# Optimization experiments

Hardware: AMD Instinct MI355X
Metric: run time of the kernel (lower is better)

The kernel has to match this reference:

```python
import jax, jax.numpy as jnp
import numpy as np

N, C_IN, C_OUT, K, S, P, H, W = 16, 64, 128, 3, 1, 1, 224, 224

def setup_inputs() -> dict:
    key = jax.random.key(0)
    kx, kw = jax.random.split(key)
    x = jax.random.normal(kx, (N, C_IN, H, W), dtype=jnp.float32)
    weight = jax.random.normal(kw, (C_OUT, C_IN, K, K), dtype=jnp.float32)
    bias = jnp.zeros((C_OUT,), dtype=jnp.float32)
    return {"x": x, "weight": weight, "bias": bias}

def reference(x, weight, bias):
    # im2col + matmul with stride 1 is exactly a standard conv2d with SAME-style padding P
    out = jax.lax.conv_general_dilated(
        x, weight,
        window_strides=(S, S),
        padding=((P, P), (P, P)),
        dimension_numbers=("NCHW", "OIHW", "NCHW"),
    )
    return out + bias[None, :, None, None]  # [N, C_OUT, H, W]
```

## Files before the change

kernel.cpp:

```cpp
#include <hip/hip_runtime.h>
#include <cstdint>
#include <cstddef>


typedef short bf16x8 __attribute__((ext_vector_type(8)));
typedef float f32x4 __attribute__((ext_vector_type(4)));

#define N_ 16
#define CI_ 64
#define CO_ 128
#define H_ 224
#define W_ 224
#define HW_ (H_ * W_)

#define WP_ 226
#define CBS_ 1808ULL
#define HPS_ 14464ULL
#define NS_ 3268864ULL

__device__ __forceinline__ unsigned short f2bf(float f) {
    unsigned u = __builtin_bit_cast(unsigned, f);
    u += 0x7FFFu + ((u >> 16) & 1u);
    return (unsigned short)(u >> 16);
}

__global__ void prep_weight(const float* __restrict__ w, unsigned short* __restrict__ wr) {
    int i = blockIdx.x * 256 + threadIdx.x;
    if (i >= 9 * CO_ * CI_) return;
    int ci = i & 63;
    int co = (i >> 6) & 127;
    int t  = i >> 13;
    wr[i] = f2bf(w[(co * CI_ + ci) * 9 + t]);
}

__global__ __launch_bounds__(256) void prep_x(const float* __restrict__ x,
                                              unsigned short* __restrict__ xp) {
    int b = blockIdx.x;
    int n = b / 226, hp = b - n * 226;
    int tid = threadIdx.x;
    unsigned short* row = xp + (size_t)n * NS_ + (size_t)hp * HPS_;
    if (hp == 0 || hp == 225) {
        #pragma unroll
        for (int k = 0; k < 8; ++k) {
            int i = k * 256 + tid;
            if (i < 1808) ((uint4*)row)[i] = make_uint4(0, 0, 0, 0);
        }
        return;
    }
    int h = hp - 1;
    const float* xb = x + (size_t)n * CI_ * HW_ + (size_t)h * W_;
    for (int k = 0; k < 7; ++k) {
        int item = k * 256 + tid;
        int w = item % 224;
        int cb = item / 224;
        unsigned r[4];
        #pragma unroll
        for (int c = 0; c < 4; ++c) {
            float lo = xb[(size_t)(cb * 8 + 2 * c) * HW_ + w];
            float hi = xb[(size_t)(cb * 8 + 2 * c + 1) * HW_ + w];
            r[c] = (unsigned)f2bf(lo) | ((unsigned)f2bf(hi) << 16);
        }
        *(uint4*)(row + (size_t)cb * CBS_ + (size_t)(w + 1) * 8) = make_uint4(r[0], r[1], r[2], r[3]);
    }
    if (tid < 16) {
        int cb = tid >> 1, wp = (tid & 1) * 225;
        *(uint4*)(row + (size_t)cb * CBS_ + (size_t)wp * 8) = make_uint4(0, 0, 0, 0);
    }
}

__global__ __launch_bounds__(512, 2) void conv2(
    const unsigned short* __restrict__ xp, const unsigned short* __restrict__ wr,
    const float* __restrict__ bias, float* __restrict__ out)
{
    __shared__ __align__(16) unsigned short xs[4 * 4 * 226 * 8];

    int bid = blockIdx.x;
    int swz = (bid & 7) * 224 + (bid >> 3);
    int n = swz / 112;
    int hblk = swz - n * 112;
    int h0 = hblk * 2;

    int tid = threadIdx.x, lane = tid & 63, wid = tid >> 6;
    int hr = wid & 1, nh = (wid >> 1) & 1, mh = wid >> 2;
    int lrow = lane & 15, lk = lane >> 4;

    f32x4 acc[4][7];
    #pragma unroll
    for (int a = 0; a < 4; ++a)
        #pragma unroll
        for (int b2 = 0; b2 < 7; ++b2)
            #pragma unroll
            for (int k = 0; k < 4; ++k)
                acc[a][b2][k] = 0.0f;

    const unsigned short* xpn = xp + (size_t)n * NS_;

    for (int ch = 0; ch < 2; ++ch) {
        if (ch) __syncthreads();
        #pragma unroll
        for (int rr = 0; rr < 2; ++rr) {
            int run = wid * 2 + rr;
            int r = run >> 2, cbl = run & 3;
            const unsigned short* src = xpn + (size_t)(h0 + r) * HPS_ + (size_t)(ch * 4 + cbl) * CBS_;
            unsigned short* dst = &xs[(size_t)(r * 4 + cbl) * (226 * 8)];
            #pragma unroll
            for (int c = 0; c < 4; ++c) {
                int chunk = c * 64 + lane;
                if (chunk < 226)
                    __builtin_amdgcn_global_load_lds(
                        (const __attribute__((address_space(1))) void*)(src + (size_t)chunk * 8),
                        (__attribute__((address_space(3))) void*)(dst + c * 512),
                        16, 0, 0);
            }
        }
        __syncthreads();

        #pragma unroll
        for (int t = 0; t < 9; ++t) {
            int kh = t / 3, kw = t - kh * 3;
            bf16x8 afr[4];
            #pragma unroll
            for (int mf = 0; mf < 4; ++mf) {
                size_t ai = ((size_t)(t * 128 + mh * 64 + mf * 16 + lrow)) * 64
                          + (size_t)(ch * 32 + lk * 8);
                afr[mf] = *(const bf16x8*)(wr + ai);
            }
            int rbase = ((hr + kh) * 4 + lk) * 226;
            int wpb = nh * 112 + lrow + kw;
            #pragma unroll
            for (int nf = 0; nf < 7; ++nf) {
                bf16x8 bfr = *(const bf16x8*)(&xs[(size_t)(rbase + wpb + nf * 16) * 8]);
                #pragma unroll
                for (int mf = 0; mf < 4; ++mf)
                    acc[mf][nf] = __builtin_amdgcn_mfma_f32_16x16x32_bf16(
                        afr[mf], bfr, acc[mf][nf], 0, 0, 0);
            }
        }
    }

    __syncthreads();
    float* lf = (float*)xs;
    int h = h0 + hr;
    #pragma unroll
    for (int mf = 0; mf < 4; ++mf) {
        float bv[4];
        #pragma unroll
        for (int r = 0; r < 4; ++r)
            bv[r] = bias[mh * 64 + mf * 16 + lk * 4 + r];
        float* wbase = lf + wid * 1808 + lk * 452 + lrow;
        #pragma unroll
        for (int r = 0; r < 4; ++r)
            #pragma unroll
            for (int nf = 0; nf < 7; ++nf)
                wbase[r * 112 + nf * 16] = acc[mf][nf][r] + bv[r];
        #pragma unroll
        for (int j = 0; j < 7; ++j) {
            int idx4 = j * 64 + lane;
            int col = idx4 / 28;
            int w4  = idx4 - col * 28;
            f32x4 v = *(const f32x4*)(lf + wid * 1808 + (col >> 2) * 452 + (col & 3) * 112 + w4 * 4);
            size_t ob = (((size_t)n * CO_ + mh * 64 + mf * 16 + col) * H_ + h) * W_
                      + nh * 112 + w4 * 4;
            *(f32x4*)(out + ob) = v;
        }
    }
}

__global__ __launch_bounds__(512, 2) void conv_mfma(
    const float* __restrict__ x, const unsigned short* __restrict__ wr,
    const float* __restrict__ bias, float* __restrict__ out)
{
    __shared__ unsigned short xs[4 * 4 * 226 * 8];
    int bid = blockIdx.x;
    int swz = (bid & 7) * 224 + (bid >> 3);
    int n = swz / 112;
    int hblk = swz - n * 112;
    int h0 = hblk * 2;
    int tid = threadIdx.x;
    int lane = tid & 63;
    int wid = tid >> 6;
    int hr = wid & 1, nh = (wid >> 1) & 1, mh = wid >> 2;
    int lrow = lane & 15, lk = lane >> 4;

    f32x4 acc[4][7];
    #pragma unroll
    for (int a = 0; a < 4; ++a)
        #pragma unroll
        for (int b = 0; b < 7; ++b)
            #pragma unroll
            for (int k = 0; k < 4; ++k)
                acc[a][b][k] = 0.0f;

    for (int ch = 0; ch < 2; ++ch) {
        if (ch) __syncthreads();
        const float* xb = x + ((size_t)n * CI_ + (size_t)ch * 32) * HW_;
        int wcol = tid % 224;
        int rem = tid / 224;
        for (int it = 0; it < 7; ++it) {
            float v[8]; int bi[8];
            #pragma unroll
            for (int u = 0; u < 8; ++u) {
                int ciL = rem & 31;
                int r4 = rem >> 5;
                int hh = h0 - 1 + r4;
                float val = 0.0f;
                if ((unsigned)hh < (unsigned)H_)
                    val = xb[(size_t)ciL * HW_ + (size_t)hh * W_ + wcol];
                v[u] = val;
                bi[u] = (((r4 << 2) + (ciL >> 3)) * 226 + wcol + 1) * 8 + (ciL & 7);
                wcol += 64; rem += 2;
                if (wcol >= 224) { wcol -= 224; rem += 1; }
            }
            #pragma unroll
            for (int u = 0; u < 8; ++u)
                xs[bi[u]] = f2bf(v[u]);
        }
        if (tid < 256) {
            int wp = (tid & 1) * 225;
            int ciL = (tid >> 1) & 31;
            int r4 = tid >> 6;
            xs[(((r4 << 2) + (ciL >> 3)) * 226 + wp) * 8 + (ciL & 7)] = 0;
        }
        __syncthreads();

        #pragma unroll
        for (int t = 0; t < 9; ++t) {
            int kh = t / 3, kw = t - kh * 3;
            bf16x8 afr[4];
            #pragma unroll
            for (int mf = 0; mf < 4; ++mf) {
                size_t ai = ((size_t)(t * 128 + mh * 64 + mf * 16 + lrow)) * 64
                          + (size_t)(ch * 32 + lk * 8);
                afr[mf] = *(const bf16x8*)(wr + ai);
            }
            int rbase = ((hr + kh) * 4 + lk) * 226;
            int wpb = nh * 112 + lrow + kw;
            #pragma unroll
            for (int nf = 0; nf < 7; ++nf) {
                bf16x8 bfr = *(const bf16x8*)(&xs[(size_t)(rbase + wpb + nf * 16) * 8]);
                #pragma unroll
                for (int mf = 0; mf < 4; ++mf)
                    acc[mf][nf] = __builtin_amdgcn_mfma_f32_16x16x32_bf16(
                        afr[mf], bfr, acc[mf][nf], 0, 0, 0);
            }
        }
    }

    int h = h0 + hr;
    #pragma unroll
    for (int mf = 0; mf < 4; ++mf) {
        #pragma unroll
        for (int r = 0; r < 4; ++r) {
            int co = mh * 64 + mf * 16 + lk * 4 + r;
            float bv = bias[co];
            size_t ob = (((size_t)n * CO_ + co) * H_ + h) * W_ + nh * 112 + lrow;
            #pragma unroll
            for (int nf = 0; nf < 7; ++nf)
                out[ob + (size_t)nf * 16] = acc[mf][nf][r] + bv;
        }
    }
}

extern "C" void kernel_launch(void* const* d_in, const int* in_sizes, int n_in,
                              void* d_out, int out_size, void* d_ws, size_t ws_size,
                              hipStream_t stream) {
    const float* x    = (const float*)d_in[0];
    const float* w    = (const float*)d_in[1];
    const float* bias = (const float*)d_in[2];
    float* out = (float*)d_out;
    unsigned short* wr = (unsigned short*)d_ws;
    const size_t xp_bytes = (size_t)N_ * NS_ * 2;
    const size_t need = 147456 + xp_bytes;

    prep_weight<<<dim3(288), dim3(256), 0, stream>>>(w, wr);
    if (ws_size >= need) {
        unsigned short* xp = wr + 73728;
        prep_x<<<dim3(16 * 226), dim3(256), 0, stream>>>(x, xp);
        conv2<<<dim3(16 * 112), dim3(512), 0, stream>>>(xp, wr, bias, out);
    } else {
        conv_mfma<<<dim3(16 * 112), dim3(512), 0, stream>>>(x, wr, bias, out);
    }
}
```

Baseline: 287.6 us.

## Split conv2 blocks by width half and load all input channels at once

Each block now covers half the output width with 256 threads instead of the full width with 512, which doubles the grid. The block loads all 8 channel groups (with halo) into LDS in one pass, removing the second load phase and its barrier. Each wave now computes a 64-channel by 112-pixel tile, so per-wave work is unchanged. The cost is that the kw halo columns are reloaded at the width split, and occupancy now depends on whether more of the smaller blocks fit per CU.

```diff
diff --git a/kernel.cpp b/kernel.cpp
--- a/kernel.cpp
+++ b/kernel.cpp
@@ -68,20 +68,22 @@
     }
 }
 
-__global__ __launch_bounds__(512, 2) void conv2(
+__global__ __launch_bounds__(256, 2) void conv2(
     const unsigned short* __restrict__ xp, const unsigned short* __restrict__ wr,
     const float* __restrict__ bias, float* __restrict__ out)
 {
-    __shared__ __align__(16) unsigned short xs[4 * 4 * 226 * 8];
+    __shared__ __align__(16) unsigned short xs[4 * 8 * 114 * 8];
 
     int bid = blockIdx.x;
-    int swz = (bid & 7) * 224 + (bid >> 3);
-    int n = swz / 112;
-    int hblk = swz - n * 112;
+    int swz = (bid & 7) * 448 + (bid >> 3);
+    int n = swz / 224;
+    int r2 = swz - n * 224;
+    int hblk = r2 >> 1;
+    int wseg = r2 & 1;
     int h0 = hblk * 2;
 
     int tid = threadIdx.x, lane = tid & 63, wid = tid >> 6;
-    int hr = wid & 1, nh = (wid >> 1) & 1, mh = wid >> 2;
+    int hr = wid & 1, mh = wid >> 1;
     int lrow = lane & 15, lk = lane >> 4;
 
     f32x4 acc[4][7];
@@ -95,26 +97,33 @@
 
     const unsigned short* xpn = xp + (size_t)n * NS_;
 
+    #pragma unroll
+    for (int it = 0; it < 14; ++it) {
+        int idx = it * 256 + tid;
+        int wp = idx % 114;
+        int rc = idx / 114;
+        const unsigned short* src = xpn + (size_t)(h0 + (rc >> 3)) * HPS_
+                                  + (size_t)(rc & 7) * CBS_ + (size_t)(wseg * 112 + wp) * 8;
+        __builtin_amdgcn_global_load_lds(
+            (const __attribute__((address_space(1))) void*)src,
+            (__attribute__((address_space(3))) void*)(xs + (size_t)idx * 8),
+            16, 0, 0);
+    }
+    if (tid < 64) {
+        int idx = 3584 + tid;
+        int wp = idx % 114;
+        int rc = idx / 114;
+        const unsigned short* src = xpn + (size_t)(h0 + (rc >> 3)) * HPS_
+                                  + (size_t)(rc & 7) * CBS_ + (size_t)(wseg * 112 + wp) * 8;
+        __builtin_amdgcn_global_load_lds(
+            (const __attribute__((address_space(1))) void*)src,
+            (__attribute__((address_space(3))) void*)(xs + (size_t)idx * 8),
+            16, 0, 0);
+    }
+    __syncthreads();
+
+    #pragma unroll
     for (int ch = 0; ch < 2; ++ch) {
-        if (ch) __syncthreads();
-        #pragma unroll
-        for (int rr = 0; rr < 2; ++rr) {
-            int run = wid * 2 + rr;
-            int r = run >> 2, cbl = run & 3;
-            const unsigned short* src = xpn + (size_t)(h0 + r) * HPS_ + (size_t)(ch * 4 + cbl) * CBS_;
-            unsigned short* dst = &xs[(size_t)(r * 4 + cbl) * (226 * 8)];
-            #pragma unroll
-            for (int c = 0; c < 4; ++c) {
-                int chunk = c * 64 + lane;
-                if (chunk < 226)
-                    __builtin_amdgcn_global_load_lds(
-                        (const __attribute__((address_space(1))) void*)(src + (size_t)chunk * 8),
-                        (__attribute__((address_space(3))) void*)(dst + c * 512),
-                        16, 0, 0);
-            }
-        }
-        __syncthreads();
-
         #pragma unroll
         for (int t = 0; t < 9; ++t) {
             int kh = t / 3, kw = t - kh * 3;
@@ -125,8 +134,8 @@
                           + (size_t)(ch * 32 + lk * 8);
                 afr[mf] = *(const bf16x8*)(wr + ai);
             }
-            int rbase = ((hr + kh) * 4 + lk) * 226;
-            int wpb = nh * 112 + lrow + kw;
+            int rbase = ((hr + kh) * 8 + ch * 4 + lk) * 114;
+            int wpb = lrow + kw;
             #pragma unroll
             for (int nf = 0; nf < 7; ++nf) {
                 bf16x8 bfr = *(const bf16x8*)(&xs[(size_t)(rbase + wpb + nf * 16) * 8]);
@@ -160,7 +169,7 @@
             int w4  = idx4 - col * 28;
             f32x4 v = *(const f32x4*)(lf + wid * 1808 + (col >> 2) * 452 + (col & 3) * 112 + w4 * 4);
             size_t ob = (((size_t)n * CO_ + mh * 64 + mf * 16 + col) * H_ + h) * W_
-                      + nh * 112 + w4 * 4;
+                      + wseg * 112 + w4 * 4;
             *(f32x4*)(out + ob) = v;
         }
     }
@@ -276,7 +285,7 @@
     if (ws_size >= need) {
         unsigned short* xp = wr + 73728;
         prep_x<<<dim3(16 * 226), dim3(256), 0, stream>>>(x, xp);
-        conv2<<<dim3(16 * 112), dim3(512), 0, stream>>>(xp, wr, bias, out);
+        conv2<<<dim3(16 * 112 * 2), dim3(256), 0, stream>>>(xp, wr, bias, out);
     } else {
         conv_mfma<<<dim3(16 * 112), dim3(512), 0, stream>>>(x, wr, bias, out);
     }
```

Result: no change. 286.5 us (-0.4%).
